# Kernel tuning notes

Hardware: AMD Instinct MI355X
Metric: run time of the kernel (lower is better)

## Reference

```python
import jax, jax.numpy as jnp
import numpy as np

B, S, D, H = 1, 2048, 2048, 32
HD = D // H
SCALE = float(HD) ** -0.5


def _rope(x, cos, sin):
    # x: (b, s, h, hd); interleaved-pair RoPE as in executorch apply_rotary_emb
    xr, xi = x[..., 0::2], x[..., 1::2]
    c = cos[None, :, None, :]
    s = sin[None, :, None, :]
    out = jnp.stack([xr * c - xi * s, xr * s + xi * c], axis=-1)
    return out.reshape(x.shape)


def setup_inputs() -> dict:
    key = jax.random.key(0)
    ks = jax.random.split(key, 8)
    hidden_states = jax.random.normal(ks[0], (B, S, D), jnp.float32)
    pos = jnp.arange(S, dtype=jnp.float32)
    inv = 1.0 / (10000.0 ** (jnp.arange(0, HD, 2, dtype=jnp.float32) / HD))
    ang = pos[:, None] * inv[None, :]  # (S, HD//2)
    freqs_cos = jnp.cos(ang)
    freqs_sin = jnp.sin(ang)
    causal = jnp.tril(jnp.ones((S, S), dtype=bool))
    attention_mask = jnp.where(causal, 0.0, -1e9).astype(jnp.float32)[None, None]
    k_cache = jax.random.normal(ks[1], (B, S, H, HD), jnp.float32)
    v_cache = jax.random.normal(ks[2], (B, S, H, HD), jnp.float32)
    k_mask = jnp.ones((B, S, 1, 1), jnp.float32)
    v_mask = jnp.ones((B, S, 1, 1), jnp.float32)
    # weights stored as (in, out); math-equivalent to torch Linear(out,in) @ W.T
    wq = jax.random.normal(ks[3], (D, D), jnp.float32) * 0.02
    wk = jax.random.normal(ks[4], (D, D), jnp.float32) * 0.02
    wv = jax.random.normal(ks[5], (D, D), jnp.float32) * 0.02
    wo = jax.random.normal(ks[6], (D, D), jnp.float32) * 0.02
    return {"hidden_states": hidden_states, "freqs_cos": freqs_cos,
            "freqs_sin": freqs_sin, "attention_mask": attention_mask,
            "k_cache": k_cache, "v_cache": v_cache,
            "k_mask": k_mask, "v_mask": v_mask,
            "wq": wq, "wk": wk, "wv": wv, "wo": wo}


def reference(hidden_states, freqs_cos, freqs_sin, attention_mask,
              k_cache, v_cache, k_mask, v_mask, wq, wk, wv, wo):
    b, s, _ = hidden_states.shape
    q = (hidden_states @ wq).reshape(b, s, H, HD)
    k = (hidden_states @ wk).reshape(b, s, H, HD)
    v = (hidden_states @ wv).reshape(b, s, H, HD)
    q = _rope(q, freqs_cos, freqs_sin)
    k = _rope(k, freqs_cos, freqs_sin)
    # mask-blend KV cache update
    k = k_cache * (1.0 - k_mask) + k * k_mask  # (b, S, H, HD)
    v = v_cache * (1.0 - v_mask) + v * v_mask
    qt = q.transpose(0, 2, 1, 3)  # (b, H, s, HD)
    kt = k.transpose(0, 2, 1, 3)
    vt = v.transpose(0, 2, 1, 3)
    attn = jnp.einsum('bhqd,bhkd->bhqk', qt, kt) * SCALE + attention_mask
    attn = jax.nn.softmax(attn, axis=-1)
    y = jnp.einsum('bhqk,bhkd->bhqd', attn, vt)  # (b, H, s, HD)
    # torch: y.transpose(0,1).contiguous().view(b, s, dim); valid since b == 1
    y = jnp.swapaxes(y, 0, 1).reshape(b, s, D)
    y = y @ wo
    return (y, k, v)
```

## Files before the change

### kernel.cpp

```cpp
#include <hip/hip_runtime.h>
#include <hip/hip_bf16.h>
#include <stdint.h>

typedef __bf16 bf16;
typedef __attribute__((ext_vector_type(8))) __bf16 bf16x8;
typedef __attribute__((ext_vector_type(4))) float f32x4;

#define SEQ 2048
#define DIM 2048
#define NHEAD 32
#define HD 64
#define SCALE_L2E 0.18033688011112042f

__device__ __forceinline__ void gload16(void* lds, const void* g) {
  __builtin_amdgcn_global_load_lds(
      (const __attribute__((address_space(1))) unsigned int*)g,
      (__attribute__((address_space(3))) unsigned int*)lds, 16, 0, 0);
}

__device__ __forceinline__ f32x4 mfma16(bf16x8 a, bf16x8 b, f32x4 c) {
  return __builtin_amdgcn_mfma_f32_16x16x32_bf16(a, b, c, 0, 0, 0);
}

__global__ __launch_bounds__(256) void prep(
    const float* __restrict__ hs, bf16* __restrict__ hsb,
    const float* __restrict__ w0, const float* __restrict__ w1,
    const float* __restrict__ w2, const float* __restrict__ w3,
    bf16* __restrict__ t0, bf16* __restrict__ t1,
    bf16* __restrict__ t2, bf16* __restrict__ t3) {
  int t = threadIdx.x;
  if (blockIdx.z == 4) {
    size_t i = ((size_t)(blockIdx.y * 32 + blockIdx.x) * 256 + t) * 16;
#pragma unroll
    for (int half = 0; half < 2; ++half) {
      f32x4 a = *(const f32x4*)(hs + i + half * 8);
      f32x4 b = *(const f32x4*)(hs + i + half * 8 + 4);
      bf16x8 o;
#pragma unroll
      for (int j = 0; j < 4; ++j) { o[j] = (bf16)a[j]; o[j + 4] = (bf16)b[j]; }
      *(bf16x8*)(hsb + i + half * 8) = o;
    }
    return;
  }
  const float* wsrc[4] = {w0, w1, w2, w3};
  bf16* wdst[4] = {t0, t1, t2, t3};
  const float* w = wsrc[blockIdx.z];
  bf16* wT = wdst[blockIdx.z];
  __shared__ alignas(16) bf16 tile[64][72];
  int n0 = blockIdx.x * 64, k0 = blockIdx.y * 64;
#pragma unroll
  for (int i = 0; i < 4; ++i) {
    int r = (t >> 4) + 16 * i;
    int c = (t & 15) * 4;
    f32x4 v = *(const f32x4*)(w + (size_t)(k0 + r) * DIM + n0 + c);
#pragma unroll
    for (int j = 0; j < 4; ++j) tile[r][c + j] = (bf16)v[j];
  }
  __syncthreads();
#pragma unroll
  for (int i = 0; i < 2; ++i) {
    int n = (t >> 3) + 32 * i;
    int kb = (t & 7) * 8;
    bf16x8 o;
#pragma unroll
    for (int j = 0; j < 8; ++j) o[j] = tile[kb + j][n];
    *(bf16x8*)(wT + (size_t)(n0 + n) * DIM + k0 + kb) = o;
  }
}

template <typename OutT>
__global__ __launch_bounds__(256) void gemm128(
    const bf16* __restrict__ A,
    const bf16* __restrict__ B0, const bf16* __restrict__ B1, const bf16* __restrict__ B2,
    OutT* __restrict__ C0, OutT* __restrict__ C1, OutT* __restrict__ C2,
    int M, int N, int K) {
  const bf16* Bt; OutT* C;
  if (blockIdx.z == 0)      { Bt = B0; C = C0; }
  else if (blockIdx.z == 1) { Bt = B1; C = C1; }
  else                      { Bt = B2; C = C2; }
  __shared__ alignas(16) bf16 As[128][64];
  __shared__ alignas(16) bf16 Bs[128][64];
  int tid = threadIdx.x, lane = tid & 63, w = tid >> 6;
  int wr = w >> 1, wc = w & 1;
  size_t mBase = (size_t)blockIdx.y * 128, nBase = (size_t)blockIdx.x * 128;
  f32x4 acc[4][4] = {};
  int r0 = tid >> 3, sl = tid & 7;
  int lr = lane & 15, hi = lane >> 4, sw = lr & 7;
  for (int kt = 0; kt < K; kt += 64) {
#pragma unroll
    for (int i = 0; i < 4; ++i) {
      int row = r0 + 32 * i;
      int kc = sl ^ (row & 7);
      gload16(&As[row][sl * 8], A + (mBase + row) * K + kt + kc * 8);
      gload16(&Bs[row][sl * 8], Bt + (nBase + row) * K + kt + kc * 8);
    }
    __syncthreads();
#pragma unroll
    for (int kk = 0; kk < 2; ++kk) {
      int cb = kk * 4 + hi;
      bf16x8 a[4], b[4];
#pragma unroll
      for (int m = 0; m < 4; ++m)
        a[m] = *(const bf16x8*)&As[wr * 64 + m * 16 + lr][(cb ^ sw) * 8];
#pragma unroll
      for (int n = 0; n < 4; ++n)
        b[n] = *(const bf16x8*)&Bs[wc * 64 + n * 16 + lr][(cb ^ sw) * 8];
#pragma unroll
      for (int m = 0; m < 4; ++m)
#pragma unroll
        for (int n = 0; n < 4; ++n)
          acc[m][n] = mfma16(a[m], b[n], acc[m][n]);
    }
    __syncthreads();
  }
#pragma unroll
  for (int m = 0; m < 4; ++m)
#pragma unroll
    for (int n = 0; n < 4; ++n)
#pragma unroll
      for (int j = 0; j < 4; ++j) {
        size_t row = mBase + wr * 64 + m * 16 + hi * 4 + j;
        size_t col = nBase + wc * 64 + n * 16 + lr;
        C[row * N + col] = (OutT)acc[m][n][j];
      }
}

__global__ __launch_bounds__(512) void gemm_out(
    const bf16* __restrict__ A, const bf16* __restrict__ Bt,
    float* __restrict__ Y) {
  const int K = DIM, N = DIM;
  __shared__ alignas(16) bf16 As[2][128][64];
  __shared__ alignas(16) bf16 Bs[2][128][64];
  __shared__ alignas(16) float red[128][132];
  int tid = threadIdx.x;
  int grp = tid >> 8;
  int gt = tid & 255;
  int lane = gt & 63, w = gt >> 6;
  int wr = w >> 1, wc = w & 1;
  size_t mBase = (size_t)blockIdx.y * 128, nBase = (size_t)blockIdx.x * 128;
  f32x4 acc[4][4] = {};
  int r0 = gt >> 3, sl = gt & 7;
  int lr = lane & 15, hi = lane >> 4, sw = lr & 7;
  int kbeg = grp * (K / 2);
  for (int kt = kbeg; kt < kbeg + K / 2; kt += 64) {
#pragma unroll
    for (int i = 0; i < 4; ++i) {
      int row = r0 + 32 * i;
      int kc = sl ^ (row & 7);
      gload16(&As[grp][row][sl * 8], A + (mBase + row) * K + kt + kc * 8);
      gload16(&Bs[grp][row][sl * 8], Bt + (nBase + row) * K + kt + kc * 8);
    }
    __syncthreads();
#pragma unroll
    for (int kk = 0; kk < 2; ++kk) {
      int cb = kk * 4 + hi;
      bf16x8 a[4], b[4];
#pragma unroll
      for (int m = 0; m < 4; ++m)
        a[m] = *(const bf16x8*)&As[grp][wr * 64 + m * 16 + lr][(cb ^ sw) * 8];
#pragma unroll
      for (int n = 0; n < 4; ++n)
        b[n] = *(const bf16x8*)&Bs[grp][wc * 64 + n * 16 + lr][(cb ^ sw) * 8];
#pragma unroll
      for (int m = 0; m < 4; ++m)
#pragma unroll
        for (int n = 0; n < 4; ++n)
          acc[m][n] = mfma16(a[m], b[n], acc[m][n]);
    }
    __syncthreads();
  }
  if (grp == 1) {
#pragma unroll
    for (int m = 0; m < 4; ++m)
#pragma unroll
      for (int n = 0; n < 4; ++n)
#pragma unroll
        for (int j = 0; j < 4; ++j)
          red[wr * 64 + m * 16 + hi * 4 + j][wc * 64 + n * 16 + lr] = acc[m][n][j];
  }
  __syncthreads();
  if (grp == 0) {
#pragma unroll
    for (int m = 0; m < 4; ++m)
#pragma unroll
      for (int n = 0; n < 4; ++n)
#pragma unroll
        for (int j = 0; j < 4; ++j) {
          int row = wr * 64 + m * 16 + hi * 4 + j;
          int col = wc * 64 + n * 16 + lr;
          Y[(mBase + row) * N + nBase + col] = acc[m][n][j] + red[row][col];
        }
  }
}

__global__ __launch_bounds__(256) void qkvprep(
    const bf16* __restrict__ qraw, const bf16* __restrict__ kraw,
    const bf16* __restrict__ vraw,
    const float* __restrict__ fc, const float* __restrict__ fs,
    const float* __restrict__ kcache, const float* __restrict__ kmask,
    const float* __restrict__ vcache, const float* __restrict__ vmask,
    float* __restrict__ kout, float* __restrict__ vout,
    bf16* __restrict__ qb, bf16* __restrict__ kb, bf16* __restrict__ vtb) {
  __shared__ alignas(16) bf16 tile[64][72];
  int bid = blockIdx.x;
  if (bid < SEQ) {
    int s = bid;
    int c0 = threadIdx.x * 8;
    int h = c0 >> 6, d0 = c0 & 63;
    float km = kmask[s], omk = 1.0f - km;
    size_t src = (size_t)s * DIM + c0;
    f32x4 cc = *(const f32x4*)(fc + s * 32 + (d0 >> 1));
    f32x4 ss = *(const f32x4*)(fs + s * 32 + (d0 >> 1));
    bf16x8 qv = *(const bf16x8*)(qraw + src);
    bf16x8 kv = *(const bf16x8*)(kraw + src);
    float kcf[8];
    *(f32x4*)(kcf) = *(const f32x4*)(kcache + src);
    *(f32x4*)(kcf + 4) = *(const f32x4*)(kcache + src + 4);
    bf16x8 qo, ko;
    float kof[8];
#pragma unroll
    for (int i = 0; i < 4; ++i) {
      float c = cc[i], sn = ss[i];
      float qr = (float)qv[2 * i], qi = (float)qv[2 * i + 1];
      qo[2 * i]     = (bf16)(qr * c - qi * sn);
      qo[2 * i + 1] = (bf16)(qr * sn + qi * c);
      float kr = (float)kv[2 * i], ki = (float)kv[2 * i + 1];
      float b0 = kcf[2 * i] * omk + (kr * c - ki * sn) * km;
      float b1 = kcf[2 * i + 1] * omk + (kr * sn + ki * c) * km;
      kof[2 * i] = b0; kof[2 * i + 1] = b1;
      ko[2 * i] = (bf16)b0; ko[2 * i + 1] = (bf16)b1;
    }
    *(f32x4*)(kout + src) = *(f32x4*)kof;
    *(f32x4*)(kout + src + 4) = *(f32x4*)(kof + 4);
    size_t dsth = ((size_t)h * SEQ + s) * HD + d0;
    *(bf16x8*)(qb + dsth) = qo;
    *(bf16x8*)(kb + dsth) = ko;
    return;
  }
  int vb = bid - SEQ;
  int h = vb >> 5;
  int s0 = (vb & 31) * 64;
  int t = threadIdx.x;
#pragma unroll
  for (int i = 0; i < 4; ++i) {
    int r = (t >> 4) + 16 * i;
    int c = (t & 15) * 4;
    int s = s0 + r;
    float vm = vmask[s], om = 1.0f - vm;
    size_t src = (size_t)s * DIM + h * 64 + c;
    f32x4 vc = *(const f32x4*)(vcache + src);
    f32x4 o;
#pragma unroll
    for (int j = 0; j < 4; ++j) {
      float val = vc[j] * om + (float)vraw[src + j] * vm;
      o[j] = val;
      tile[r][c + j] = (bf16)val;
    }
    *(f32x4*)(vout + src) = o;
  }
  __syncthreads();
#pragma unroll
  for (int i = 0; i < 2; ++i) {
    int hd = (t >> 3) + 32 * i;
    int cb = (t & 7) * 8;
    bf16x8 o;
#pragma unroll
    for (int j = 0; j < 8; ++j) o[j] = tile[cb + j][hd];
    *(bf16x8*)(vtb + (size_t)h * HD * SEQ + (size_t)hd * SEQ + s0 + cb) = o;
  }
}

__global__ __launch_bounds__(512) void attn_fwd(
    const bf16* __restrict__ qb, const bf16* __restrict__ kb,
    const bf16* __restrict__ vtb, bf16* __restrict__ ob) {
  int orig = blockIdx.x;
  int wg = (orig & 7) * 32 + (orig >> 3);
  int h = wg >> 3;
  int qp = wg & 7;
  int qtA = qp, qtB = 15 - qp;
  int ntA = qtA + 1;
  const int NT = 17;
  __shared__ alignas(16) bf16 Ks[128][64];
  __shared__ alignas(16) bf16 Vs[64][128];
  __shared__ alignas(16) bf16 Ps[8][16][128];
  int tid = threadIdx.x, lane = tid & 63, w = tid >> 6;
  const bf16* qh = qb + (size_t)h * SEQ * HD;
  const bf16* kh = kb + (size_t)h * SEQ * HD;
  const bf16* vh = vtb + (size_t)h * HD * SEQ;
  int lr = lane & 15, hi = lane >> 4, sw = lr & 7;
  int qrowA = qtA * 128 + w * 16 + lr;
  int qrowB = qtB * 128 + w * 16 + lr;
  bf16x8 qfA[2], qfB[2];
#pragma unroll
  for (int kk = 0; kk < 2; ++kk) {
    qfA[kk] = *(const bf16x8*)(qh + (size_t)qrowA * HD + kk * 32 + hi * 8);
    qfB[kk] = *(const bf16x8*)(qh + (size_t)qrowB * HD + kk * 32 + hi * 8);
  }
  f32x4 otA[4] = {}, otB[4] = {};
  float mA = -3e38f, lA = 0.f, mB = -3e38f, lB = 0.f;
  char* PsW = (char*)&Ps[w][0][0];

  auto STAGE = [&](int kv0) {
    int kr0 = tid >> 3, ksl = tid & 7;
#pragma unroll
    for (int i = 0; i < 2; ++i) {
      int row = kr0 + 64 * i;
      int kc = ksl ^ (row & 7);
      gload16(&Ks[row][ksl * 8], kh + (size_t)(kv0 + row) * HD + kc * 8);
    }
    int vr0 = tid >> 4, vsl = tid & 15;
#pragma unroll
    for (int i = 0; i < 2; ++i) {
      int row = vr0 + 32 * i;
      int vc = vsl ^ (row & 7);
      gload16(&Vs[row][vsl * 8], vh + (size_t)row * SEQ + kv0 + vc * 8);
    }
  };

  auto BODY = [&](int kv0, bf16x8 (&qf)[2], f32x4 (&ot)[4],
                  float& mrun, float& lrun, int qrow, bool last) {
    f32x4 st[8] = {};
    __builtin_amdgcn_s_setprio(1);
#pragma unroll
    for (int kk = 0; kk < 2; ++kk) {
      int cb = kk * 4 + hi;
#pragma unroll
      for (int n = 0; n < 8; ++n) {
        bf16x8 kf = *(const bf16x8*)&Ks[n * 16 + lr][(cb ^ sw) * 8];
        st[n] = mfma16(kf, qf[kk], st[n]);
      }
    }
    __builtin_amdgcn_s_setprio(0);
    if (last) {
#pragma unroll
      for (int n = 0; n < 8; ++n)
#pragma unroll
        for (int j = 0; j < 4; ++j) {
          int key = kv0 + n * 16 + hi * 4 + j;
          st[n][j] = (key <= qrow) ? st[n][j] * SCALE_L2E : -1e30f;
        }
    } else {
#pragma unroll
      for (int n = 0; n < 8; ++n)
#pragma unroll
        for (int j = 0; j < 4; ++j) st[n][j] *= SCALE_L2E;
    }
    float tm[8];
#pragma unroll
    for (int n = 0; n < 8; ++n)
      tm[n] = fmaxf(fmaxf(st[n][0], st[n][1]), fmaxf(st[n][2], st[n][3]));
    float t01 = fmaxf(tm[0], tm[1]), t23 = fmaxf(tm[2], tm[3]);
    float t45 = fmaxf(tm[4], tm[5]), t67 = fmaxf(tm[6], tm[7]);
    float tmax = fmaxf(fmaxf(t01, t23), fmaxf(t45, t67));
    tmax = fmaxf(tmax, __shfl_xor(tmax, 16));
    tmax = fmaxf(tmax, __shfl_xor(tmax, 32));
    if (!__all(tmax <= mrun + 8.f)) {
      float mnew = fmaxf(mrun, tmax);
      float alpha = exp2f(mrun - mnew);
      mrun = mnew;
      lrun *= alpha;
#pragma unroll
      for (int nd = 0; nd < 4; ++nd)
#pragma unroll
        for (int j = 0; j < 4; ++j) ot[nd][j] *= alpha;
    }
    float ps[8];
#pragma unroll
    for (int n = 0; n < 8; ++n) {
      float p0 = exp2f(st[n][0] - mrun), p1 = exp2f(st[n][1] - mrun);
      float p2 = exp2f(st[n][2] - mrun), p3 = exp2f(st[n][3] - mrun);
      st[n][0] = p0; st[n][1] = p1; st[n][2] = p2; st[n][3] = p3;
      ps[n] = (p0 + p1) + (p2 + p3);
    }
    float psum = ((ps[0] + ps[1]) + (ps[2] + ps[3])) +
                 ((ps[4] + ps[5]) + (ps[6] + ps[7]));
    psum += __shfl_xor(psum, 16);
    psum += __shfl_xor(psum, 32);
    lrun += psum;
#pragma unroll
    for (int n = 0; n < 8; ++n) {
      union { bf16 b[4]; uint2 u; } pk;
#pragma unroll
      for (int j = 0; j < 4; ++j) pk.b[j] = (bf16)st[n][j];
      int keyc = n * 2 + (hi >> 1);
      *(uint2*)(PsW + lr * 256 + ((keyc ^ sw) * 16) + (hi & 1) * 8) = pk.u;
    }
    __builtin_amdgcn_s_setprio(1);
#pragma unroll
    for (int kk = 0; kk < 4; ++kk) {
      int cb = kk * 4 + hi;
      bf16x8 pf = *(const bf16x8*)(PsW + lr * 256 + ((cb ^ sw) * 16));
#pragma unroll
      for (int nd = 0; nd < 4; ++nd) {
        bf16x8 vf = *(const bf16x8*)&Vs[nd * 16 + lr][(cb ^ sw) * 8];
        ot[nd] = mfma16(vf, pf, ot[nd]);
      }
    }
    __builtin_amdgcn_s_setprio(0);
  };

  auto STORE = [&](f32x4 (&ot)[4], float lrun, int qrow) {
    float rinv = 1.0f / lrun;
    bf16* orow = ob + ((size_t)h * SEQ + qrow) * HD;
#pragma unroll
    for (int nd = 0; nd < 4; ++nd) {
      union { bf16 b[4]; uint2 u; } o;
#pragma unroll
      for (int j = 0; j < 4; ++j) o.b[j] = (bf16)(ot[nd][j] * rinv);
      *(uint2*)(orow + nd * 16 + hi * 4) = o.u;
    }
  };

  STAGE(0);
  for (int t = 0; t < NT; ++t) {
    __syncthreads();
    if (t < ntA) {
      int kv0 = t * 128;
      BODY(kv0, qfA, otA, mA, lA, qrowA, t == ntA - 1);
      if (t == ntA - 1) STORE(otA, lA, qrowA);
    } else {
      int kv0 = (t - ntA) * 128;
      BODY(kv0, qfB, otB, mB, lB, qrowB, t == NT - 1);
    }
    __syncthreads();
    if (t + 1 < NT) {
      int tn = t + 1;
      int kvn = (tn < ntA ? tn : tn - ntA) * 128;
      STAGE(kvn);
    }
  }
  STORE(otB, lB, qrowB);
}

extern "C" void kernel_launch(void* const* d_in, const int* in_sizes, int n_in,
                              void* d_out, int out_size, void* d_ws, size_t ws_size,
                              hipStream_t stream) {
  const float* hs     = (const float*)d_in[0];
  const float* fc     = (const float*)d_in[1];
  const float* fs     = (const float*)d_in[2];
  const float* kcache = (const float*)d_in[4];
  const float* vcache = (const float*)d_in[5];
  const float* kmask  = (const float*)d_in[6];
  const float* vmask  = (const float*)d_in[7];
  const float* wq     = (const float*)d_in[8];
  const float* wk     = (const float*)d_in[9];
  const float* wv     = (const float*)d_in[10];
  const float* wo     = (const float*)d_in[11];

  float* y    = (float*)d_out;
  float* kout = y + (size_t)SEQ * DIM;
  float* vout = y + 2 * (size_t)SEQ * DIM;

  char* ws = (char*)d_ws;
  const size_t MB8 = (size_t)SEQ * DIM * sizeof(bf16);
  bf16* wqT  = (bf16*)(ws + 0 * MB8);
  bf16* wkT  = (bf16*)(ws + 1 * MB8);
  bf16* wvT  = (bf16*)(ws + 2 * MB8);
  bf16* woT  = (bf16*)(ws + 3 * MB8);
  bf16* hsb  = (bf16*)(ws + 4 * MB8);
  bf16* qraw = (bf16*)(ws + 5 * MB8);
  bf16* kraw = (bf16*)(ws + 6 * MB8);
  bf16* vraw = (bf16*)(ws + 7 * MB8);
  bf16* qb   = (bf16*)(ws + 8 * MB8);
  bf16* kb   = (bf16*)(ws + 9 * MB8);
  bf16* vtb  = (bf16*)(ws + 10 * MB8);
  bf16* ob   = hsb;

  prep<<<dim3(32, 32, 5), dim3(256), 0, stream>>>(
      hs, hsb, wq, wk, wv, wo, wqT, wkT, wvT, woT);
  gemm128<bf16><<<dim3(16, 16, 3), dim3(256), 0, stream>>>(
      hsb, wqT, wkT, wvT, qraw, kraw, vraw, SEQ, DIM, DIM);
  qkvprep<<<dim3(SEQ + 1024), dim3(256), 0, stream>>>(
      qraw, kraw, vraw, fc, fs, kcache, kmask, vcache, vmask,
      kout, vout, qb, kb, vtb);
  attn_fwd<<<dim3(256), dim3(512), 0, stream>>>(qb, kb, vtb, ob);
  gemm_out<<<dim3(16, 16), dim3(512), 0, stream>>>(ob, woT, y);
}
```

Before: 187.4 us.

## Give each attention wave two 16-row query groups with 256-thread blocks

The attention kernel drops from 8 waves to 4 waves per block. Each wave now handles 32 query rows as two 16-row groups, so every K and V fragment read from LDS feeds two MFMAs. This halves LDS fragment traffic per MFMA and spreads staging over fewer threads, each issuing more loads. In exchange, register pressure roughly doubles for accumulators and scores, and there are fewer waves per block to hide latency.

```diff
diff --git a/kernel.cpp b/kernel.cpp
--- a/kernel.cpp
+++ b/kernel.cpp
@@ -270,7 +270,7 @@
   }
 }
 
-__global__ __launch_bounds__(512) void attn_fwd(
+__global__ __launch_bounds__(256) void attn_fwd(
     const bf16* __restrict__ qb, const bf16* __restrict__ kb,
     const bf16* __restrict__ vtb, bf16* __restrict__ ob) {
   int orig = blockIdx.x;
@@ -282,44 +282,49 @@
   const int NT = 17;
   __shared__ alignas(16) bf16 Ks[128][64];
   __shared__ alignas(16) bf16 Vs[64][128];
-  __shared__ alignas(16) bf16 Ps[8][16][128];
+  __shared__ alignas(16) bf16 Ps[4][32][128];
   int tid = threadIdx.x, lane = tid & 63, w = tid >> 6;
   const bf16* qh = qb + (size_t)h * SEQ * HD;
   const bf16* kh = kb + (size_t)h * SEQ * HD;
   const bf16* vh = vtb + (size_t)h * HD * SEQ;
   int lr = lane & 15, hi = lane >> 4, sw = lr & 7;
-  int qrowA = qtA * 128 + w * 16 + lr;
-  int qrowB = qtB * 128 + w * 16 + lr;
-  bf16x8 qfA[2], qfB[2];
-#pragma unroll
-  for (int kk = 0; kk < 2; ++kk) {
-    qfA[kk] = *(const bf16x8*)(qh + (size_t)qrowA * HD + kk * 32 + hi * 8);
-    qfB[kk] = *(const bf16x8*)(qh + (size_t)qrowB * HD + kk * 32 + hi * 8);
-  }
-  f32x4 otA[4] = {}, otB[4] = {};
-  float mA = -3e38f, lA = 0.f, mB = -3e38f, lB = 0.f;
+  int qrowA[2], qrowB[2];
+  bf16x8 qfA[2][2], qfB[2][2];
+#pragma unroll
+  for (int g = 0; g < 2; ++g) {
+    qrowA[g] = qtA * 128 + w * 32 + g * 16 + lr;
+    qrowB[g] = qtB * 128 + w * 32 + g * 16 + lr;
+#pragma unroll
+    for (int kk = 0; kk < 2; ++kk) {
+      qfA[g][kk] = *(const bf16x8*)(qh + (size_t)qrowA[g] * HD + kk * 32 + hi * 8);
+      qfB[g][kk] = *(const bf16x8*)(qh + (size_t)qrowB[g] * HD + kk * 32 + hi * 8);
+    }
+  }
+  f32x4 otA[2][4] = {}, otB[2][4] = {};
+  float mA[2] = {-3e38f, -3e38f}, lA[2] = {0.f, 0.f};
+  float mB[2] = {-3e38f, -3e38f}, lB[2] = {0.f, 0.f};
   char* PsW = (char*)&Ps[w][0][0];
 
   auto STAGE = [&](int kv0) {
     int kr0 = tid >> 3, ksl = tid & 7;
 #pragma unroll
-    for (int i = 0; i < 2; ++i) {
-      int row = kr0 + 64 * i;
+    for (int i = 0; i < 4; ++i) {
+      int row = kr0 + 32 * i;
       int kc = ksl ^ (row & 7);
       gload16(&Ks[row][ksl * 8], kh + (size_t)(kv0 + row) * HD + kc * 8);
     }
     int vr0 = tid >> 4, vsl = tid & 15;
 #pragma unroll
-    for (int i = 0; i < 2; ++i) {
-      int row = vr0 + 32 * i;
+    for (int i = 0; i < 4; ++i) {
+      int row = vr0 + 16 * i;
       int vc = vsl ^ (row & 7);
       gload16(&Vs[row][vsl * 8], vh + (size_t)row * SEQ + kv0 + vc * 8);
     }
   };
 
-  auto BODY = [&](int kv0, bf16x8 (&qf)[2], f32x4 (&ot)[4],
-                  float& mrun, float& lrun, int qrow, bool last) {
-    f32x4 st[8] = {};
+  auto BODY = [&](int kv0, bf16x8 (&qf)[2][2], f32x4 (&ot)[2][4],
+                  float (&mrun)[2], float (&lrun)[2], int* qrow, bool last) {
+    f32x4 st[2][8] = {};
     __builtin_amdgcn_s_setprio(1);
 #pragma unroll
     for (int kk = 0; kk < 2; ++kk) {
@@ -327,87 +332,97 @@
 #pragma unroll
       for (int n = 0; n < 8; ++n) {
         bf16x8 kf = *(const bf16x8*)&Ks[n * 16 + lr][(cb ^ sw) * 8];
-        st[n] = mfma16(kf, qf[kk], st[n]);
+        st[0][n] = mfma16(kf, qf[0][kk], st[0][n]);
+        st[1][n] = mfma16(kf, qf[1][kk], st[1][n]);
       }
     }
     __builtin_amdgcn_s_setprio(0);
-    if (last) {
+#pragma unroll
+    for (int g = 0; g < 2; ++g) {
+      if (last) {
+#pragma unroll
+        for (int n = 0; n < 8; ++n)
+#pragma unroll
+          for (int j = 0; j < 4; ++j) {
+            int key = kv0 + n * 16 + hi * 4 + j;
+            st[g][n][j] = (key <= qrow[g]) ? st[g][n][j] * SCALE_L2E : -1e30f;
+          }
+      } else {
+#pragma unroll
+        for (int n = 0; n < 8; ++n)
+#pragma unroll
+          for (int j = 0; j < 4; ++j) st[g][n][j] *= SCALE_L2E;
+      }
+      float tm[8];
 #pragma unroll
       for (int n = 0; n < 8; ++n)
-#pragma unroll
-        for (int j = 0; j < 4; ++j) {
-          int key = kv0 + n * 16 + hi * 4 + j;
-          st[n][j] = (key <= qrow) ? st[n][j] * SCALE_L2E : -1e30f;
-        }
-    } else {
-#pragma unroll
-      for (int n = 0; n < 8; ++n)
-#pragma unroll
-        for (int j = 0; j < 4; ++j) st[n][j] *= SCALE_L2E;
-    }
-    float tm[8];
-#pragma unroll
-    for (int n = 0; n < 8; ++n)
-      tm[n] = fmaxf(fmaxf(st[n][0], st[n][1]), fmaxf(st[n][2], st[n][3]));
-    float t01 = fmaxf(tm[0], tm[1]), t23 = fmaxf(tm[2], tm[3]);
-    float t45 = fmaxf(tm[4], tm[5]), t67 = fmaxf(tm[6], tm[7]);
-    float tmax = fmaxf(fmaxf(t01, t23), fmaxf(t45, t67));
-    tmax = fmaxf(tmax, __shfl_xor(tmax, 16));
-    tmax = fmaxf(tmax, __shfl_xor(tmax, 32));
-    if (!__all(tmax <= mrun + 8.f)) {
-      float mnew = fmaxf(mrun, tmax);
-      float alpha = exp2f(mrun - mnew);
-      mrun = mnew;
-      lrun *= alpha;
-#pragma unroll
-      for (int nd = 0; nd < 4; ++nd)
-#pragma unroll
-        for (int j = 0; j < 4; ++j) ot[nd][j] *= alpha;
-    }
-    float ps[8];
-#pragma unroll
-    for (int n = 0; n < 8; ++n) {
-      float p0 = exp2f(st[n][0] - mrun), p1 = exp2f(st[n][1] - mrun);
-      float p2 = exp2f(st[n][2] - mrun), p3 = exp2f(st[n][3] - mrun);
-      st[n][0] = p0; st[n][1] = p1; st[n][2] = p2; st[n][3] = p3;
-      ps[n] = (p0 + p1) + (p2 + p3);
-    }
-    float psum = ((ps[0] + ps[1]) + (ps[2] + ps[3])) +
-                 ((ps[4] + ps[5]) + (ps[6] + ps[7]));
-    psum += __shfl_xor(psum, 16);
-    psum += __shfl_xor(psum, 32);
-    lrun += psum;
-#pragma unroll
-    for (int n = 0; n < 8; ++n) {
-      union { bf16 b[4]; uint2 u; } pk;
-#pragma unroll
-      for (int j = 0; j < 4; ++j) pk.b[j] = (bf16)st[n][j];
-      int keyc = n * 2 + (hi >> 1);
-      *(uint2*)(PsW + lr * 256 + ((keyc ^ sw) * 16) + (hi & 1) * 8) = pk.u;
+        tm[n] = fmaxf(fmaxf(st[g][n][0], st[g][n][1]),
+                      fmaxf(st[g][n][2], st[g][n][3]));
+      float t01 = fmaxf(tm[0], tm[1]), t23 = fmaxf(tm[2], tm[3]);
+      float t45 = fmaxf(tm[4], tm[5]), t67 = fmaxf(tm[6], tm[7]);
+      float tmax = fmaxf(fmaxf(t01, t23), fmaxf(t45, t67));
+      tmax = fmaxf(tmax, __shfl_xor(tmax, 16));
+      tmax = fmaxf(tmax, __shfl_xor(tmax, 32));
+      if (!__all(tmax <= mrun[g] + 8.f)) {
+        float mnew = fmaxf(mrun[g], tmax);
+        float alpha = exp2f(mrun[g] - mnew);
+        mrun[g] = mnew;
+        lrun[g] *= alpha;
+#pragma unroll
+        for (int nd = 0; nd < 4; ++nd)
+#pragma unroll
+          for (int j = 0; j < 4; ++j) ot[g][nd][j] *= alpha;
+      }
+      float ps[8];
+#pragma unroll
+      for (int n = 0; n < 8; ++n) {
+        float p0 = exp2f(st[g][n][0] - mrun[g]), p1 = exp2f(st[g][n][1] - mrun[g]);
+        float p2 = exp2f(st[g][n][2] - mrun[g]), p3 = exp2f(st[g][n][3] - mrun[g]);
+        st[g][n][0] = p0; st[g][n][1] = p1; st[g][n][2] = p2; st[g][n][3] = p3;
+        ps[n] = (p0 + p1) + (p2 + p3);
+      }
+      float psum = ((ps[0] + ps[1]) + (ps[2] + ps[3])) +
+                   ((ps[4] + ps[5]) + (ps[6] + ps[7]));
+      psum += __shfl_xor(psum, 16);
+      psum += __shfl_xor(psum, 32);
+      lrun[g] += psum;
+#pragma unroll
+      for (int n = 0; n < 8; ++n) {
+        union { bf16 b[4]; uint2 u; } pk;
+#pragma unroll
+        for (int j = 0; j < 4; ++j) pk.b[j] = (bf16)st[g][n][j];
+        int keyc = n * 2 + (hi >> 1);
+        *(uint2*)(PsW + (g * 16 + lr) * 256 + ((keyc ^ sw) * 16) + (hi & 1) * 8) = pk.u;
+      }
     }
     __builtin_amdgcn_s_setprio(1);
 #pragma unroll
     for (int kk = 0; kk < 4; ++kk) {
       int cb = kk * 4 + hi;
-      bf16x8 pf = *(const bf16x8*)(PsW + lr * 256 + ((cb ^ sw) * 16));
+      bf16x8 pf0 = *(const bf16x8*)(PsW + lr * 256 + ((cb ^ sw) * 16));
+      bf16x8 pf1 = *(const bf16x8*)(PsW + (16 + lr) * 256 + ((cb ^ sw) * 16));
 #pragma unroll
       for (int nd = 0; nd < 4; ++nd) {
         bf16x8 vf = *(const bf16x8*)&Vs[nd * 16 + lr][(cb ^ sw) * 8];
-        ot[nd] = mfma16(vf, pf, ot[nd]);
+        ot[0][nd] = mfma16(vf, pf0, ot[0][nd]);
+        ot[1][nd] = mfma16(vf, pf1, ot[1][nd]);
       }
     }
     __builtin_amdgcn_s_setprio(0);
   };
 
-  auto STORE = [&](f32x4 (&ot)[4], float lrun, int qrow) {
-    float rinv = 1.0f / lrun;
-    bf16* orow = ob + ((size_t)h * SEQ + qrow) * HD;
-#pragma unroll
-    for (int nd = 0; nd < 4; ++nd) {
-      union { bf16 b[4]; uint2 u; } o;
-#pragma unroll
-      for (int j = 0; j < 4; ++j) o.b[j] = (bf16)(ot[nd][j] * rinv);
-      *(uint2*)(orow + nd * 16 + hi * 4) = o.u;
+  auto STORE = [&](f32x4 (&ot)[2][4], float (&lrun)[2], int* qrow) {
+#pragma unroll
+    for (int g = 0; g < 2; ++g) {
+      float rinv = 1.0f / lrun[g];
+      bf16* orow = ob + ((size_t)h * SEQ + qrow[g]) * HD;
+#pragma unroll
+      for (int nd = 0; nd < 4; ++nd) {
+        union { bf16 b[4]; uint2 u; } o;
+#pragma unroll
+        for (int j = 0; j < 4; ++j) o.b[j] = (bf16)(ot[g][nd][j] * rinv);
+        *(uint2*)(orow + nd * 16 + hi * 4) = o.u;
+      }
     }
   };
 
@@ -473,6 +488,6 @@
   qkvprep<<<dim3(SEQ + 1024), dim3(256), 0, stream>>>(
       qraw, kraw, vraw, fc, fs, kcache, kmask, vcache, vmask,
       kout, vout, qb, kb, vtb);
-  attn_fwd<<<dim3(256), dim3(512), 0, stream>>>(qb, kb, vtb, ob);
+  attn_fwd<<<dim3(256), dim3(256), 0, stream>>>(qb, kb, vtb, ob);
   gemm_out<<<dim3(16, 16), dim3(512), 0, stream>>>(ob, woT, y);
 }
```

Result: slower. 197.0 us (+5.1%).
